# Optimization experiments

Measured on AMD Instinct MI355X. Metric: run time of the kernel, lower is better.

The kernel has to match this reference:

```python
import math
import jax, jax.numpy as jnp
import numpy as np

HEADS = 16


def setup_inputs() -> dict:
    key = jax.random.key(0)
    k1, k2, k3, k4, k5 = jax.random.split(key, 5)
    B, S, D = 2, 2048, 1024
    return {
        "x": jax.random.normal(k1, (B, S, D), dtype=jnp.float32),
        "Wqkv": jax.random.normal(k2, (3 * D, D), dtype=jnp.float32) * (1.0 / math.sqrt(D)),
        "bqkv": jax.random.normal(k3, (3 * D,), dtype=jnp.float32) * 0.02,
        "Wo": jax.random.normal(k4, (D, D), dtype=jnp.float32) * (1.0 / math.sqrt(D)),
        "bo": jax.random.normal(k5, (D,), dtype=jnp.float32) * 0.02,
    }


def reference(x, Wqkv, bqkv, Wo, bo):
    B, S, D = x.shape
    H = HEADS
    hd = D // H  # head dim
    qkv = x @ Wqkv.T + bqkv                      # (B, S, 3D)
    # Faithful to torch: direct contiguous reshape (NOT a transpose-based head split)
    qkv = qkv.reshape(B, H, S, 3 * hd)           # (B, H, S, 3*hd)
    q, k, v = jnp.split(qkv, 3, axis=-1)         # each (B, H, S, hd)
    scores = jnp.einsum("bhsd,bhtd->bhst", q, k) * (1.0 / math.sqrt(hd))
    attn = jax.nn.softmax(scores, axis=-1)       # (B, H, S, S)
    vals = jnp.einsum("bhst,bhtd->bhsd", attn, v)
    vals = vals.reshape(B, S, D)                 # faithful direct reshape back
    return vals @ Wo.T + bo
```

## Files before the change

kernel.cpp:

```cpp
#include <hip/hip_runtime.h>
#include <stdint.h>

typedef unsigned short u16;
typedef __attribute__((ext_vector_type(8))) short short8;
typedef __attribute__((ext_vector_type(4))) float f32x4;
typedef __attribute__((ext_vector_type(16))) float f32x16;
typedef __attribute__((ext_vector_type(8))) __bf16 bf16x8;
typedef __attribute__((ext_vector_type(4))) unsigned u32x4;

#define DEV static __device__ __forceinline__

template <typename T>
DEV auto mfma_try(T a, T b, f32x4 c, int)
    -> decltype(__builtin_amdgcn_mfma_f32_16x16x32_bf16(a, b, c, 0, 0, 0)) {
  return __builtin_amdgcn_mfma_f32_16x16x32_bf16(a, b, c, 0, 0, 0);
}
template <typename T>
DEV f32x4 mfma_try(T a, T b, f32x4 c, long) {
  return __builtin_amdgcn_mfma_f32_16x16x32_bf16(
      __builtin_bit_cast(bf16x8, a), __builtin_bit_cast(bf16x8, b), c, 0, 0, 0);
}
DEV f32x4 MFMA(short8 a, short8 b, f32x4 c) { return mfma_try(a, b, c, 0); }

template <typename T>
DEV auto mfma32_try(T a, T b, f32x16 c, int)
    -> decltype(__builtin_amdgcn_mfma_f32_32x32x16_bf16(a, b, c, 0, 0, 0)) {
  return __builtin_amdgcn_mfma_f32_32x32x16_bf16(a, b, c, 0, 0, 0);
}
template <typename T>
DEV f32x16 mfma32_try(T a, T b, f32x16 c, long) {
  return __builtin_amdgcn_mfma_f32_32x32x16_bf16(
      __builtin_bit_cast(bf16x8, a), __builtin_bit_cast(bf16x8, b), c, 0, 0, 0);
}
DEV f32x16 MFMA32(short8 a, short8 b, f32x16 c) { return mfma32_try(a, b, c, 0); }

DEV void gload16(const u16* g, u16* lds) {
  __builtin_amdgcn_global_load_lds((unsigned int*)g, (unsigned int*)lds, 16, 0, 0);
}

DEV u16 f2bf(float f) {
  unsigned u = __float_as_uint(f);
  u = (u + 0x7FFFu + ((u >> 16) & 1u)) >> 16;
  return (u16)u;
}

DEV float exp2fast(float x) {
  float r;
  asm("v_exp_f32 %0, %1" : "=v"(r) : "v"(x));
  return r;
}

DEV unsigned cvtpk_bf16(float lo, float hi_) {
  unsigned r;
  asm("v_cvt_pk_bf16_f32 %0, %1, %2" : "=v"(r) : "v"(lo), "v"(hi_));
  return r;
}

DEV void permswap(unsigned& a, unsigned& b) {
  asm volatile("v_permlane32_swap_b32 %0, %1" : "+v"(a), "+v"(b));
}

__global__ void cvt_kernel(const float* __restrict__ x, const float* __restrict__ wq,
                           const float* __restrict__ wo, u16* __restrict__ xb,
                           u16* __restrict__ wqb, u16* __restrict__ wob) {
  const int N1 = 4194304 / 4, N2 = 3145728 / 4, N3 = 1048576 / 4;
  const int total = N1 + N2 + N3;
  for (int i = blockIdx.x * blockDim.x + threadIdx.x; i < total;
       i += gridDim.x * blockDim.x) {
    const float4* s;
    u16* d;
    int off;
    if (i < N1) { s = (const float4*)x; d = xb; off = i; }
    else if (i < N1 + N2) { s = (const float4*)wq; d = wqb; off = i - N1; }
    else { s = (const float4*)wo; d = wob; off = i - N1 - N2; }
    float4 v = s[off];
    ushort4 o;
    o.x = f2bf(v.x); o.y = f2bf(v.y); o.z = f2bf(v.z); o.w = f2bf(v.w);
    ((ushort4*)d)[off] = o;
  }
}

__global__ __launch_bounds__(256, 4) void gemm1_128(
    const u16* __restrict__ A, const u16* __restrict__ Bm,
    const float* __restrict__ bias,
    u16* __restrict__ Qb, u16* __restrict__ Kb, u16* __restrict__ Vb) {
  __shared__ u16 SM[128 * 136];
  u16* const As = SM;
  u16* const Bs = SM + 4096;
  const int K = 1024;
  const int tid = threadIdx.x;
  const int lane = tid & 63;
  const int wave = tid >> 6;
  const int wr = wave >> 1, wc = wave & 1;
  const int l15 = lane & 15, l4 = lane >> 4;
  const int m0 = blockIdx.y * 128, n0 = blockIdx.x * 128;

  f32x4 acc[4][4] = {};

  const u16* ga = A + (size_t)(m0 + (tid >> 2)) * K + (tid & 3) * 8;
  const u16* gb = Bm + (size_t)(n0 + (tid >> 2)) * K + (tid & 3) * 8;
  u16* la = As + tid * 8;
  u16* lb = Bs + tid * 8;
  const size_t rstep = (size_t)64 * K;

  for (int kt = 0; kt < K; kt += 32) {
    gload16(ga + kt, la);
    gload16(ga + kt + rstep, la + 2048);
    gload16(gb + kt, lb);
    gload16(gb + kt + rstep, lb + 2048);
    __syncthreads();
    short8 af[4], bfr[4];
#pragma unroll
    for (int i = 0; i < 4; ++i)
      af[i] = *(const short8*)(As + (wr * 64 + i * 16 + l15) * 32 + l4 * 8);
#pragma unroll
    for (int i = 0; i < 4; ++i)
      bfr[i] = *(const short8*)(Bs + (wc * 64 + i * 16 + l15) * 32 + l4 * 8);
#pragma unroll
    for (int i = 0; i < 4; ++i)
#pragma unroll
      for (int j = 0; j < 4; ++j) acc[i][j] = MFMA(af[i], bfr[j], acc[i][j]);
    __syncthreads();
  }

#pragma unroll
  for (int nj = 0; nj < 4; ++nj) {
    const int cl = wc * 64 + nj * 16 + l15;
    const float bv = bias[n0 + cl];
#pragma unroll
    for (int mi = 0; mi < 4; ++mi)
#pragma unroll
      for (int r = 0; r < 4; ++r) {
        const int ml = wr * 64 + mi * 16 + l4 * 4 + r;
        SM[ml * 136 + cl] = f2bf(acc[mi][nj][r] + bv);
      }
  }
  __syncthreads();

  const int ml = tid >> 1;
  const int h = tid & 1;
  const int m = m0 + ml;
  const int c0 = n0 + h * 64;
  const int chunk = c0 / 192;
  const int sel = (c0 - chunk * 192) >> 6;
  u16* const dst = (sel == 0) ? Qb : ((sel == 1) ? Kb : Vb);
  const int s = m & 2047;
  const int bh = (m >> 11) * 16 + (s >> 7);
  const int s2 = (s & 127) * 16 + chunk;
  u16* const drow = dst + ((size_t)bh * 2048 + s2) * 64;
  const u16* const srow = SM + ml * 136 + h * 64;
#pragma unroll
  for (int g = 0; g < 8; ++g)
    *(short8*)(drow + g * 8) = *(const short8*)(srow + g * 8);
}

__global__ __launch_bounds__(256, 2) void gemm_bt(
    const u16* __restrict__ A, const u16* __restrict__ Bm,
    const float* __restrict__ bias, float* __restrict__ Cf, int M, int N, int K) {
  __shared__ u16 As[128 * 32];
  __shared__ u16 Bs[128 * 32];
  const int tid = threadIdx.x;
  const int lane = tid & 63;
  const int wave = tid >> 6;
  const int wr = wave >> 1, wc = wave & 1;
  const int l15 = lane & 15, l4 = lane >> 4;
  const int m0 = blockIdx.y * 128, n0 = blockIdx.x * 128;

  f32x4 acc[4][4] = {};

  const u16* ga = A + (size_t)(m0 + (tid >> 2)) * K + (tid & 3) * 8;
  const u16* gb = Bm + (size_t)(n0 + (tid >> 2)) * K + (tid & 3) * 8;
  u16* la = As + tid * 8;
  u16* lb = Bs + tid * 8;
  const size_t rstep = (size_t)64 * K;

  for (int kt = 0; kt < K; kt += 32) {
    gload16(ga + kt, la);
    gload16(ga + kt + rstep, la + 2048);
    gload16(gb + kt, lb);
    gload16(gb + kt + rstep, lb + 2048);
    __syncthreads();
    short8 af[4], bfr[4];
#pragma unroll
    for (int i = 0; i < 4; ++i)
      af[i] = *(const short8*)(As + (wr * 64 + i * 16 + l15) * 32 + l4 * 8);
#pragma unroll
    for (int i = 0; i < 4; ++i)
      bfr[i] = *(const short8*)(Bs + (wc * 64 + i * 16 + l15) * 32 + l4 * 8);
#pragma unroll
    for (int i = 0; i < 4; ++i)
#pragma unroll
      for (int j = 0; j < 4; ++j) acc[i][j] = MFMA(af[i], bfr[j], acc[i][j]);
    __syncthreads();
  }

#pragma unroll
  for (int nj = 0; nj < 4; ++nj) {
    const int c = n0 + wc * 64 + nj * 16 + l15;
    const float bv = bias[c];
#pragma unroll
    for (int mi = 0; mi < 4; ++mi)
#pragma unroll
      for (int r = 0; r < 4; ++r) {
        const int m = m0 + wr * 64 + mi * 16 + l4 * 4 + r;
        Cf[(size_t)m * N + c] = acc[mi][nj][r] + bv;
      }
  }
}

__global__ __launch_bounds__(256) void vtrans_kernel(const u16* __restrict__ Vn,
                                                     u16* __restrict__ VT) {
  __shared__ u16 T[64 * 72];
  const int tid = threadIdx.x;
  const int bh = blockIdx.x >> 5;
  const int s0 = (blockIdx.x & 31) * 64;
  const int r = tid >> 3, c8 = tid & 7;
#pragma unroll
  for (int i = 0; i < 2; ++i) {
    const int s = r + i * 32;
    short8 v = *(const short8*)(Vn + ((size_t)bh * 2048 + s0 + s) * 64 + c8 * 8);
#pragma unroll
    for (int j = 0; j < 8; ++j) T[(c8 * 8 + j) * 72 + s] = (u16)v[j];
  }
  __syncthreads();
#pragma unroll
  for (int i = 0; i < 2; ++i) {
    const int d = (tid >> 3) + i * 32;
    short8 v = *(const short8*)(&T[d * 72 + (tid & 7) * 8]);
    *(short8*)(VT + ((size_t)bh * 64 + d) * 2048 + s0 + (tid & 7) * 8) = v;
  }
}

__global__ __launch_bounds__(512) void attn_kernel(
    const u16* __restrict__ Qg, const u16* __restrict__ Kg,
    const u16* __restrict__ VTg, u16* __restrict__ v2) {
  __shared__ __align__(16) char smem[65536];
  u16* const KS = (u16*)smem;
  u16* const VS = (u16*)smem + 16384;
  float* const FM = (float*)smem;

  const int tid = threadIdx.x;
  const int lane = tid & 63;
  const int half = tid >> 8;
  const int tid256 = tid & 255;
  const int w4 = (tid >> 6) & 3;
  const int l31 = lane & 31;
  const int hi = lane >> 5;

  const int bid = blockIdx.x;
  const int logical = (bid & 7) * 64 + (bid >> 3);
  const int bh = logical >> 4;
  const int qt = logical & 15;

  const u16* Qh = Qg + (size_t)bh * 2048 * 64;
  const u16* Kh = Kg + (size_t)bh * 2048 * 64;
  const u16* VTh = VTg + (size_t)bh * 64 * 2048;

  const int q0 = qt * 128 + w4 * 32;
  const float C1 = 0.18033688f;

  short8 qf[4];
#pragma unroll
  for (int d_ = 0; d_ < 4; ++d_)
    qf[d_] = *(const short8*)(Qh + (size_t)(q0 + l31) * 64 + d_ * 16 + hi * 8);

  f32x16 ot[2] = {};
  float ls4[4] = {0.f, 0.f, 0.f, 0.f};

  const int r8 = tid256 >> 3;
  const int c16 = tid256 & 7;
  const int xr = l31 & 7;
  const int Tbase = half * 16;

  auto stage = [&](int buf, int T) {
    u16* kd = KS + (half * 2 + buf) * 4096 + tid256 * 8;
    u16* vd = VS + (half * 2 + buf) * 4096 + tid256 * 8;
#pragma unroll
    for (int i = 0; i < 2; ++i) {
      const int row = i * 32 + r8;
      gload16(Kh + (size_t)(T * 64 + row) * 64 + ((c16 ^ (row & 7)) * 8),
              kd + i * 2048);
    }
#pragma unroll
    for (int i = 0; i < 2; ++i) {
      const int d = i * 32 + r8;
      gload16(VTh + (size_t)d * 2048 + T * 64 + ((c16 ^ (d & 7)) * 8),
              vd + i * 2048);
    }
  };

  stage(0, Tbase);
  __syncthreads();

  for (int t = 0; t < 16; ++t) {
    const int cur = t & 1;
    if (t + 1 < 16) stage(cur ^ 1, Tbase + t + 1);

    const u16* Kb = KS + (half * 2 + cur) * 4096;
    const u16* Vb = VS + (half * 2 + cur) * 4096;

    f32x16 st[2] = {};
    __builtin_amdgcn_s_setprio(1);
#pragma unroll
    for (int n = 0; n < 2; ++n)
#pragma unroll
      for (int d_ = 0; d_ < 4; ++d_) {
        short8 kf = *(const short8*)(Kb + (n * 32 + l31) * 64 +
                                     (((d_ * 2 + hi) ^ xr) * 8));
        st[n] = MFMA32(kf, qf[d_], st[n]);
      }
    __builtin_amdgcn_s_setprio(0);

    float p0[16], p1[16];
#pragma unroll
    for (int r = 0; r < 16; ++r) {
      p0[r] = exp2fast(st[0][r] * C1);
      p1[r] = exp2fast(st[1][r] * C1);
    }
#pragma unroll
    for (int i = 0; i < 4; ++i)
      ls4[i] += ((p0[i] + p0[i + 4]) + (p0[i + 8] + p0[i + 12])) +
                ((p1[i] + p1[i + 4]) + (p1[i + 8] + p1[i + 12]));

    short8 pf[2][2];
#pragma unroll
    for (int n = 0; n < 2; ++n) {
      const float* p = n ? p1 : p0;
      unsigned W[4][2];
#pragma unroll
      for (int j = 0; j < 4; ++j)
#pragma unroll
        for (int pp = 0; pp < 2; ++pp)
          W[j][pp] = cvtpk_bf16(p[4 * j + 2 * pp], p[4 * j + 2 * pp + 1]);
#pragma unroll
      for (int ks = 0; ks < 2; ++ks) {
        unsigned x0 = W[2 * ks][0], y0 = W[2 * ks + 1][0];
        unsigned x1 = W[2 * ks][1], y1 = W[2 * ks + 1][1];
        permswap(x0, y0);
        permswap(x1, y1);
        u32x4 pw = {x0, x1, y0, y1};
        pf[n][ks] = __builtin_bit_cast(short8, pw);
      }
    }

    __builtin_amdgcn_s_setprio(1);
#pragma unroll
    for (int db = 0; db < 2; ++db)
#pragma unroll
      for (int ksg = 0; ksg < 4; ++ksg) {
        short8 vf = *(const short8*)(Vb + (db * 32 + l31) * 64 +
                                     (((ksg * 2 + hi) ^ xr) * 8));
        ot[db] = MFMA32(vf, pf[ksg >> 1][ksg & 1], ot[db]);
      }
    __builtin_amdgcn_s_setprio(0);

    __syncthreads();
  }

  float l = (ls4[0] + ls4[1]) + (ls4[2] + ls4[3]);
  l += __shfl_xor(l, 32);

  if (half == 1) {
    float* F = FM + (size_t)(w4 * 64 + lane) * 33;
#pragma unroll
    for (int r = 0; r < 16; ++r) {
      F[r] = ot[0][r];
      F[16 + r] = ot[1][r];
    }
    F[32] = l;
  }
  __syncthreads();
  if (half == 0) {
    const float* F = FM + (size_t)(w4 * 64 + lane) * 33;
    const float inv = 1.0f / (l + F[32]);

    const int s2v = q0 + l31;
    const int rowO = (bh >> 4) * 2048 + (bh & 15) * 128 + (s2v >> 4);
    const int colb = (s2v & 15) * 64;
#pragma unroll
    for (int db = 0; db < 2; ++db)
#pragma unroll
      for (int g = 0; g < 4; ++g) {
        ushort4 w;
        w.x = f2bf((ot[db][4 * g + 0] + F[db * 16 + 4 * g + 0]) * inv);
        w.y = f2bf((ot[db][4 * g + 1] + F[db * 16 + 4 * g + 1]) * inv);
        w.z = f2bf((ot[db][4 * g + 2] + F[db * 16 + 4 * g + 2]) * inv);
        w.w = f2bf((ot[db][4 * g + 3] + F[db * 16 + 4 * g + 3]) * inv);
        const int d = db * 32 + 8 * g + 4 * hi;
        *(ushort4*)(v2 + (size_t)rowO * 1024 + colb + d) = w;
      }
  }
}

extern "C" void kernel_launch(void* const* d_in, const int* in_sizes, int n_in,
                              void* d_out, int out_size, void* d_ws, size_t ws_size,
                              hipStream_t stream) {
  const float* x = (const float*)d_in[0];
  const float* Wqkv = (const float*)d_in[1];
  const float* bqkv = (const float*)d_in[2];
  const float* Wo = (const float*)d_in[3];
  const float* bo = (const float*)d_in[4];
  float* out = (float*)d_out;

  char* ws = (char*)d_ws;
  u16* xb   = (u16*)(ws);
  u16* wqb  = (u16*)(ws + 8388608);
  u16* wob  = (u16*)(ws + 14680064);
  u16* Qb   = (u16*)(ws + 16777216);
  u16* Kb   = (u16*)(ws + 25165824);
  u16* VTb  = (u16*)(ws + 33554432);
  u16* v2   = (u16*)(ws + 41943040);
  u16* Vnat = v2;

  cvt_kernel<<<2048, 256, 0, stream>>>(x, Wqkv, Wo, xb, wqb, wob);

  dim3 g1(24, 32);
  gemm1_128<<<g1, 256, 0, stream>>>(xb, wqb, bqkv, Qb, Kb, Vnat);

  vtrans_kernel<<<1024, 256, 0, stream>>>(Vnat, VTb);

  attn_kernel<<<512, 512, 0, stream>>>(Qb, Kb, VTb, v2);

  dim3 g2(8, 32);
  gemm_bt<<<g2, 256, 0, stream>>>(v2, wob, bo, out, 4096, 1024, 1024);
}
```

Before: 124.4 us.

## Load V fragments directly from global memory instead of staging through LDS

Result: slower. 149.7 us (+20.3%).

```diff
diff --git a/kernel.cpp b/kernel.cpp
--- a/kernel.cpp
+++ b/kernel.cpp
@@ -231,12 +231,11 @@
   }
 }
 
-__global__ __launch_bounds__(512) void attn_kernel(
+__global__ __launch_bounds__(512, 4) void attn_kernel(
     const u16* __restrict__ Qg, const u16* __restrict__ Kg,
     const u16* __restrict__ VTg, u16* __restrict__ v2) {
-  __shared__ __align__(16) char smem[65536];
+  __shared__ __align__(16) char smem[34816];
   u16* const KS = (u16*)smem;
-  u16* const VS = (u16*)smem + 16384;
   float* const FM = (float*)smem;
 
   const int tid = threadIdx.x;
@@ -272,21 +271,16 @@
   const int xr = l31 & 7;
   const int Tbase = half * 16;
 
+  const u16* const vrow0 = VTh + (size_t)l31 * 2048 + hi * 8;
+
   auto stage = [&](int buf, int T) {
     u16* kd = KS + (half * 2 + buf) * 4096 + tid256 * 8;
-    u16* vd = VS + (half * 2 + buf) * 4096 + tid256 * 8;
 #pragma unroll
     for (int i = 0; i < 2; ++i) {
       const int row = i * 32 + r8;
       gload16(Kh + (size_t)(T * 64 + row) * 64 + ((c16 ^ (row & 7)) * 8),
               kd + i * 2048);
     }
-#pragma unroll
-    for (int i = 0; i < 2; ++i) {
-      const int d = i * 32 + r8;
-      gload16(VTh + (size_t)d * 2048 + T * 64 + ((c16 ^ (d & 7)) * 8),
-              vd + i * 2048);
-    }
   };
 
   stage(0, Tbase);
@@ -297,7 +291,7 @@
     if (t + 1 < 16) stage(cur ^ 1, Tbase + t + 1);
 
     const u16* Kb = KS + (half * 2 + cur) * 4096;
-    const u16* Vb = VS + (half * 2 + cur) * 4096;
+    const int kv0 = (Tbase + t) * 64;
 
     f32x16 st[2] = {};
     __builtin_amdgcn_s_setprio(1);
@@ -311,27 +305,25 @@
       }
     __builtin_amdgcn_s_setprio(0);
 
-    float p0[16], p1[16];
 #pragma unroll
     for (int r = 0; r < 16; ++r) {
-      p0[r] = exp2fast(st[0][r] * C1);
-      p1[r] = exp2fast(st[1][r] * C1);
+      st[0][r] = exp2fast(st[0][r] * C1);
+      st[1][r] = exp2fast(st[1][r] * C1);
     }
 #pragma unroll
     for (int i = 0; i < 4; ++i)
-      ls4[i] += ((p0[i] + p0[i + 4]) + (p0[i + 8] + p0[i + 12])) +
-                ((p1[i] + p1[i + 4]) + (p1[i + 8] + p1[i + 12]));
+      ls4[i] += ((st[0][i] + st[0][i + 4]) + (st[0][i + 8] + st[0][i + 12])) +
+                ((st[1][i] + st[1][i + 4]) + (st[1][i + 8] + st[1][i + 12]));
 
     short8 pf[2][2];
 #pragma unroll
     for (int n = 0; n < 2; ++n) {
-      const float* p = n ? p1 : p0;
       unsigned W[4][2];
 #pragma unroll
       for (int j = 0; j < 4; ++j)
 #pragma unroll
         for (int pp = 0; pp < 2; ++pp)
-          W[j][pp] = cvtpk_bf16(p[4 * j + 2 * pp], p[4 * j + 2 * pp + 1]);
+          W[j][pp] = cvtpk_bf16(st[n][4 * j + 2 * pp], st[n][4 * j + 2 * pp + 1]);
 #pragma unroll
       for (int ks = 0; ks < 2; ++ks) {
         unsigned x0 = W[2 * ks][0], y0 = W[2 * ks + 1][0];
@@ -343,16 +335,19 @@
       }
     }
 
-    __builtin_amdgcn_s_setprio(1);
-#pragma unroll
-    for (int db = 0; db < 2; ++db)
-#pragma unroll
-      for (int ksg = 0; ksg < 4; ++ksg) {
-        short8 vf = *(const short8*)(Vb + (db * 32 + l31) * 64 +
-                                     (((ksg * 2 + hi) ^ xr) * 8));
-        ot[db] = MFMA32(vf, pf[ksg >> 1][ksg & 1], ot[db]);
-      }
-    __builtin_amdgcn_s_setprio(0);
+#pragma unroll
+    for (int db = 0; db < 2; ++db) {
+      const u16* vr = vrow0 + (size_t)db * 32 * 2048 + kv0;
+      short8 vf[4];
+#pragma unroll
+      for (int ksg = 0; ksg < 4; ++ksg)
+        vf[ksg] = *(const short8*)(vr + ksg * 16);
+      __builtin_amdgcn_s_setprio(1);
+#pragma unroll
+      for (int ksg = 0; ksg < 4; ++ksg)
+        ot[db] = MFMA32(vf[ksg], pf[ksg >> 1][ksg & 1], ot[db]);
+      __builtin_amdgcn_s_setprio(0);
+    }
 
     __syncthreads();
   }
```
